# Kernel tuning notes

Hardware: AMD Instinct MI355X
Metric: run time of the kernel (lower is better)

## Reference

```python
import jax, jax.numpy as jnp
import numpy as np

B, H, L, N = 16, 256, 4096, 64


def setup_inputs() -> dict:
    key = jax.random.key(0)
    k_u, k_c, k_s = jax.random.split(key, 3)
    u = jax.random.normal(k_u, (B, H, L), dtype=jnp.float32)
    # HiPPO-style S4D-Lin init, replicated per channel
    A_re = -0.5 * jnp.ones((H, N), dtype=jnp.float32)
    A_im = jnp.pi * jnp.broadcast_to(jnp.arange(N, dtype=jnp.float32), (H, N))
    C = jax.random.normal(k_c, (H, N, 2), dtype=jnp.float32) * (0.5 ** 0.5)
    D = jnp.ones((H, 1), dtype=jnp.float32)
    log_step = jax.random.uniform(
        k_s, (H, 1), dtype=jnp.float32,
        minval=jnp.log(0.001), maxval=jnp.log(0.1))
    return {"u": u, "A_re": A_re, "A_im": A_im, "C": C, "D": D,
            "log_step": log_step}


def reference(u, A_re, A_im, C, D, log_step):
    # u: [B,H,L]; per-channel S4D params: A_* [H,N], C [H,N,2], D/log_step [H,1]
    Lq = u.shape[-1]
    step = jnp.exp(log_step)                       # [H,1]
    A = jnp.clip(A_re, None, -0.0001) + 1j * A_im  # [H,N] complex
    dtA = step * A                                 # [H,N]
    Cc = C[..., 0] + 1j * C[..., 1]                # [H,N]
    # ZOH kernel: K[h,l] = Re( sum_n C (exp(step*A)-1)/A * exp(l*step*A) )
    coef = Cc * (jnp.exp(dtA) - 1.0) / A           # [H,N]
    phase = jnp.arange(Lq)[None, :, None] * dtA[:, None, :]  # [H,L,N]
    K = jnp.einsum('hn,hln->hl', coef, jnp.exp(phase)).real  # [H,L]
    # FFT causal convolution (zero-padded to 2L)
    n = 2 * Lq
    ud = jnp.fft.rfft(u, n=n, axis=-1)             # [B,H,n//2+1]
    Kd = jnp.fft.rfft(K, n=n, axis=-1)             # [H,n//2+1]
    y = jnp.fft.irfft(ud * Kd[None], n=n, axis=-1)[..., :Lq]
    return y + D * u
```

## Files before the change

### kernel.cpp

```cpp
#include <hip/hip_runtime.h>
#include <hip/hip_bf16.h>
#include <math.h>


#define B_ 16
#define H_ 256
#define L_ 4096

typedef __attribute__((ext_vector_type(8))) short short8;
typedef __attribute__((ext_vector_type(4))) float f32x4;

#define WIN_STRIDE 72
#define TK_STRIDE  72
#define WOUT_STRIDE 136

#define WIN_ELEMS  (128 * WIN_STRIDE)
#define TK_ELEMS   (64 * TK_STRIDE)
#define WOUT_ELEMS (64 * WOUT_STRIDE)

__device__ __forceinline__ unsigned short f2bf(float f) {
    unsigned int u = __float_as_uint(f);
    u = (u + 0x7FFFu + ((u >> 16) & 1u)) >> 16;
    return (unsigned short)u;
}
__device__ __forceinline__ float bf2f(unsigned short h) {
    return __uint_as_float(((unsigned int)h) << 16);
}
__device__ __forceinline__ void split2(float v, short& hi, short& lo) {
    unsigned short h = f2bf(v);
    hi = (short)h;
    lo = (short)f2bf(v - bf2f(h));
}

__global__ __launch_bounds__(512) void s4d_tables(
    const float* __restrict__ A_re, const float* __restrict__ A_im,
    const float* __restrict__ C,    const float* __restrict__ log_step,
    unsigned short* __restrict__ win_g, unsigned short* __restrict__ tk_g,
    unsigned short* __restrict__ wout_g, float* __restrict__ lamT_g)
{
    const int bid0 = blockIdx.x;
    const int slot = bid0 >> 3;
    const int h   = (bid0 & 7) * 32 + (slot >> 4);
    const int sub = slot & 15;
    const int tid = threadIdx.x;
    __shared__ float pr[64], pi[64], cr_[64], ci_[64], Kd[64];
    __shared__ float kpart[8][64];
    const float step = expf(log_step[h]);

    if (tid < 64) {
        int n = tid;
        float are = fminf(A_re[h * 64 + n], -1e-4f);
        float aim = A_im[h * 64 + n];
        float dre = step * are, dim = step * aim;
        float er = expf(dre);
        float l1r = er * cosf(dim), l1i = er * sinf(dim);
        float inv = 1.0f / (are * are + aim * aim);
        float nre = l1r - 1.0f, nim = l1i;
        float qre = (nre * are + nim * aim) * inv;
        float qim = (nim * are - nre * aim) * inv;
        float c0 = C[(h * 64 + n) * 2], c1 = C[(h * 64 + n) * 2 + 1];
        pr[n] = dre; pi[n] = dim;
        cr_[n] = c0 * qre - c1 * qim;
        ci_[n] = c0 * qim + c1 * qre;
        if (sub == 0) {
            float m = expf(64.0f * dre);
            lamT_g[(h * 64 + n) * 2]     = m * cosf(64.0f * dim);
            lamT_g[(h * 64 + n) * 2 + 1] = m * sinf(64.0f * dim);
        }
    }
    __syncthreads();

    {
        const int d = tid & 63, q = tid >> 6;
        float acc = 0.f;
        for (int n = q * 8; n < q * 8 + 8; ++n) {
            float m = expf((float)d * pr[n]);
            float a = (float)d * pi[n];
            acc += m * (cr_[n] * cosf(a) - ci_[n] * sinf(a));
        }
        kpart[q][d] = acc;
    }
    __syncthreads();
    if (tid < 64) {
        float s01 = kpart[0][tid] + kpart[1][tid];
        float s23 = kpart[2][tid] + kpart[3][tid];
        float s45 = kpart[4][tid] + kpart[5][tid];
        float s67 = kpart[6][tid] + kpart[7][tid];
        Kd[tid] = ((s01 + s23) + s45) + s67;
    }

    unsigned short* winH = win_g + (size_t)h * (2 * WIN_ELEMS);
    unsigned short* winL = winH + WIN_ELEMS;
    for (int i = sub * 576 + tid; i < (sub + 1) * 576; i += 512) {
        int p = i / WIN_STRIDE, j = i - p * WIN_STRIDE;
        float v = 0.f;
        if (j < 64) {
            int n = p & 63;
            float e = (float)(63 - j);
            float m = expf(e * pr[n]), a = e * pi[n];
            v = (p < 64) ? m * cosf(a) : m * sinf(a);
        }
        unsigned short hv = f2bf(v);
        winH[i] = hv;
        winL[i] = f2bf(v - bf2f(hv));
    }

    unsigned short* woH = wout_g + (size_t)h * (2 * WOUT_ELEMS);
    unsigned short* woL = woH + WOUT_ELEMS;
    for (int i = sub * 544 + tid; i < (sub + 1) * 544; i += 512) {
        int j = i / WOUT_STRIDE, p = i - j * WOUT_STRIDE;
        float v = 0.f;
        if (p < 128) {
            int n = p & 63;
            float e = (float)(j + 1);
            float m = expf(e * pr[n]), a = e * pi[n];
            float lr = m * cosf(a), li = m * sinf(a);
            float wr = cr_[n] * lr - ci_[n] * li;
            float wi = cr_[n] * li + ci_[n] * lr;
            v = (p < 64) ? wr : -wi;
        }
        unsigned short hv = f2bf(v);
        woH[i] = hv;
        woL[i] = f2bf(v - bf2f(hv));
    }
    __syncthreads();

    unsigned short* tkH = tk_g + (size_t)h * (2 * TK_ELEMS);
    unsigned short* tkL = tkH + TK_ELEMS;
    for (int i = sub * 288 + tid; i < (sub + 1) * 288; i += 512) {
        int j = i / TK_STRIDE, m = i - j * TK_STRIDE;
        float v = (m < 64 && m <= j) ? Kd[j - m] : 0.f;
        unsigned short hv = f2bf(v);
        tkH[i] = hv;
        tkL[i] = f2bf(v - bf2f(hv));
    }
}

__global__ __launch_bounds__(512, 1) void s4d_main(
    const float* __restrict__ u, const float* __restrict__ D,
    const unsigned short* __restrict__ win_g, const unsigned short* __restrict__ tk_g,
    const unsigned short* __restrict__ wout_g, const float* __restrict__ lamT_g,
    float* __restrict__ y)
{
    const int tid  = threadIdx.x;
    const int lane = tid & 63, w = tid >> 6;
    const int wg   = w >> 2, ww = w & 3;
    const int l15  = lane & 15;

    const int bid  = blockIdx.x;
    const int xcd  = bid & 7, slot = bid >> 3;
    const int h  = xcd * 32 + (slot >> 3);
    const int bp = slot & 7;
    const size_t ubase0 = ((size_t)bp * H_ + h) * (size_t)L_;
    const size_t ubase1 = ((size_t)(bp + 8) * H_ + h) * (size_t)L_;

    __shared__ __align__(16) float u_lds[2][64][68];
    __shared__ __align__(16) float ES[2][64][132];
    __shared__ __align__(16) unsigned short bufB[2 * (WIN_ELEMS + TK_ELEMS)];
    unsigned short* winB  = bufB;
    unsigned short* tkB   = bufB + 2 * WIN_ELEMS;
    unsigned short* woutB = bufB;

    for (int it = 0; it < 4; ++it) {
        int l = it * 2048 + tid * 4;
        int seq = l >> 12, within = l & 4095;
        const size_t ub = seq ? ubase1 : ubase0;
        float4 v = *(const float4*)&u[ub + within];
        *(float4*)&u_lds[seq][within >> 6][within & 63] = v;
    }
    {
        const uint4* src = (const uint4*)(win_g + (size_t)h * (2 * WIN_ELEMS));
        uint4* dst = (uint4*)winB;
        for (int i = tid; i < (2 * WIN_ELEMS) / 8; i += 512) dst[i] = src[i];
    }
    {
        const uint4* src = (const uint4*)(tk_g + (size_t)h * (2 * TK_ELEMS));
        uint4* dst = (uint4*)tkB;
        for (int i = tid; i < (2 * TK_ELEMS) / 8; i += 512) dst[i] = src[i];
    }
    __syncthreads();

    const int row  = ww * 16 + l15;
    const int koff = (lane >> 4) * 8;

    short8 auh[2], aul[2];
#pragma unroll
    for (int kb = 0; kb < 2; ++kb) {
        float4 v0 = *(const float4*)&u_lds[wg][row][kb * 32 + koff];
        float4 v1 = *(const float4*)&u_lds[wg][row][kb * 32 + koff + 4];
        float vv[8] = {v0.x, v0.y, v0.z, v0.w, v1.x, v1.y, v1.z, v1.w};
#pragma unroll
        for (int e = 0; e < 8; ++e) { short hi, lo; split2(vv[e], hi, lo); auh[kb][e] = hi; aul[kb][e] = lo; }
    }

    for (int nt = 0; nt < 8; ++nt) {
        f32x4 acc = {0.f, 0.f, 0.f, 0.f};
#pragma unroll
        for (int kb = 0; kb < 2; ++kb) {
            const int boff = (nt * 16 + l15) * WIN_STRIDE + kb * 32 + koff;
            short8 bh = *(const short8*)&winB[boff];
            short8 bl = *(const short8*)&winB[WIN_ELEMS + boff];
            acc = __builtin_amdgcn_mfma_f32_16x16x32_bf16(auh[kb], bh, acc, 0, 0, 0);
            acc = __builtin_amdgcn_mfma_f32_16x16x32_bf16(aul[kb], bh, acc, 0, 0, 0);
            acc = __builtin_amdgcn_mfma_f32_16x16x32_bf16(auh[kb], bl, acc, 0, 0, 0);
        }
#pragma unroll
        for (int r = 0; r < 4; ++r)
            ES[wg][ww * 16 + (lane >> 4) * 4 + r][nt * 16 + l15] = acc[r];
    }

    f32x4 yacc[4];
    for (int nt = 0; nt < 4; ++nt) {
        f32x4 acc = {0.f, 0.f, 0.f, 0.f};
#pragma unroll
        for (int kb = 0; kb < 2; ++kb) {
            const int boff = (nt * 16 + l15) * TK_STRIDE + kb * 32 + koff;
            short8 bh = *(const short8*)&tkB[boff];
            short8 bl = *(const short8*)&tkB[TK_ELEMS + boff];
            acc = __builtin_amdgcn_mfma_f32_16x16x32_bf16(auh[kb], bh, acc, 0, 0, 0);
            acc = __builtin_amdgcn_mfma_f32_16x16x32_bf16(aul[kb], bh, acc, 0, 0, 0);
            acc = __builtin_amdgcn_mfma_f32_16x16x32_bf16(auh[kb], bl, acc, 0, 0, 0);
        }
        yacc[nt] = acc;
    }
    __syncthreads();

    if (ww == 0) {
        float ltr = lamT_g[(h * 64 + lane) * 2];
        float lti = lamT_g[(h * 64 + lane) * 2 + 1];
        float sr = 0.f, si = 0.f;
#pragma unroll 8
        for (int c = 0; c < 64; ++c) {
            float er = ES[wg][c][lane], ei = ES[wg][c][lane + 64];
            ES[wg][c][lane] = sr; ES[wg][c][lane + 64] = si;
            float nsr = ltr * sr - lti * si + er;
            si = ltr * si + lti * sr + ei;
            sr = nsr;
        }
    } else {
        const uint4* src = (const uint4*)(wout_g + (size_t)h * (2 * WOUT_ELEMS));
        uint4* dst = (uint4*)woutB;
        const int compact = (wg * 3 + (ww - 1)) * 64 + lane;
        for (int i = compact; i < (2 * WOUT_ELEMS) / 8; i += 384) dst[i] = src[i];
    }
    __syncthreads();

    for (int kb = 0; kb < 4; ++kb) {
        float4 v0 = *(const float4*)&ES[wg][row][kb * 32 + koff];
        float4 v1 = *(const float4*)&ES[wg][row][kb * 32 + koff + 4];
        float vv[8] = {v0.x, v0.y, v0.z, v0.w, v1.x, v1.y, v1.z, v1.w};
        short8 ash, asl;
#pragma unroll
        for (int e = 0; e < 8; ++e) { short hi, lo; split2(vv[e], hi, lo); ash[e] = hi; asl[e] = lo; }
#pragma unroll
        for (int nt = 0; nt < 4; ++nt) {
            const int boff = (nt * 16 + l15) * WOUT_STRIDE + kb * 32 + koff;
            short8 bh = *(const short8*)&woutB[boff];
            short8 bl = *(const short8*)&woutB[WOUT_ELEMS + boff];
            yacc[nt] = __builtin_amdgcn_mfma_f32_16x16x32_bf16(ash, bh, yacc[nt], 0, 0, 0);
            yacc[nt] = __builtin_amdgcn_mfma_f32_16x16x32_bf16(asl, bh, yacc[nt], 0, 0, 0);
            yacc[nt] = __builtin_amdgcn_mfma_f32_16x16x32_bf16(ash, bl, yacc[nt], 0, 0, 0);
        }
    }
    __syncthreads();

#pragma unroll
    for (int nt = 0; nt < 4; ++nt)
#pragma unroll
        for (int r = 0; r < 4; ++r)
            ES[wg][ww * 16 + (lane >> 4) * 4 + r][nt * 16 + l15] = yacc[nt][r];
    __syncthreads();

    const float Dh = D[h];
    for (int it = 0; it < 4; ++it) {
        int l = it * 2048 + tid * 4;
        int seq = l >> 12, within = l & 4095;
        int c = within >> 6, j = within & 63;
        float4 yv = *(const float4*)&ES[seq][c][j];
        float4 uv = *(const float4*)&u_lds[seq][c][j];
        float4 o;
        o.x = yv.x + Dh * uv.x; o.y = yv.y + Dh * uv.y;
        o.z = yv.z + Dh * uv.z; o.w = yv.w + Dh * uv.w;
        *(float4*)&y[(seq ? ubase1 : ubase0) + within] = o;
    }
}

extern "C" void kernel_launch(void* const* d_in, const int* in_sizes, int n_in,
                              void* d_out, int out_size, void* d_ws, size_t ws_size,
                              hipStream_t stream) {
    const float* u        = (const float*)d_in[0];
    const float* A_re     = (const float*)d_in[1];
    const float* A_im     = (const float*)d_in[2];
    const float* C        = (const float*)d_in[3];
    const float* D        = (const float*)d_in[4];
    const float* log_step = (const float*)d_in[5];
    float* y = (float*)d_out;

    char* ws = (char*)d_ws;
    unsigned short* win_g  = (unsigned short*)(ws);
    unsigned short* tk_g   = (unsigned short*)(ws + 9437184);
    unsigned short* wout_g = (unsigned short*)(ws + 14155776);
    float*          lamT_g = (float*)(ws + 23068672);

    s4d_tables<<<H_ * 16, 512, 0, stream>>>(A_re, A_im, C, log_step, win_g, tk_g, wout_g, lamT_g);
    s4d_main<<<(B_ * H_) / 2, 512, 0, stream>>>(u, D, win_g, tk_g, wout_g, lamT_g, y);
}
```

Before: 125.2 us.

## Fuse table generation into main kernel, computing win/tk/wout tables in LDS

```diff
diff --git a/kernel.cpp b/kernel.cpp
--- a/kernel.cpp
+++ b/kernel.cpp
@@ -32,21 +32,43 @@
     lo = (short)f2bf(v - bf2f(h));
 }
 
-__global__ __launch_bounds__(512) void s4d_tables(
+__global__ __launch_bounds__(512, 1) void s4d_main(
+    const float* __restrict__ u,
     const float* __restrict__ A_re, const float* __restrict__ A_im,
-    const float* __restrict__ C,    const float* __restrict__ log_step,
-    unsigned short* __restrict__ win_g, unsigned short* __restrict__ tk_g,
-    unsigned short* __restrict__ wout_g, float* __restrict__ lamT_g)
+    const float* __restrict__ C,    const float* __restrict__ D,
+    const float* __restrict__ log_step,
+    float* __restrict__ y)
 {
-    const int bid0 = blockIdx.x;
-    const int slot = bid0 >> 3;
-    const int h   = (bid0 & 7) * 32 + (slot >> 4);
-    const int sub = slot & 15;
-    const int tid = threadIdx.x;
+    const int tid  = threadIdx.x;
+    const int lane = tid & 63, w = tid >> 6;
+    const int wg   = w >> 2, ww = w & 3;
+    const int l15  = lane & 15;
+
+    const int bid  = blockIdx.x;
+    const int xcd  = bid & 7, slot = bid >> 3;
+    const int h  = xcd * 32 + (slot >> 3);
+    const int bp = slot & 7;
+    const size_t ubase0 = ((size_t)bp * H_ + h) * (size_t)L_;
+    const size_t ubase1 = ((size_t)(bp + 8) * H_ + h) * (size_t)L_;
+
+    __shared__ __align__(16) float u_lds[2][64][68];
+    __shared__ __align__(16) float ES[2][64][132];
+    __shared__ __align__(16) unsigned short bufB[2 * (WIN_ELEMS + TK_ELEMS)];
     __shared__ float pr[64], pi[64], cr_[64], ci_[64], Kd[64];
-    __shared__ float kpart[8][64];
+    unsigned short* winB  = bufB;
+    unsigned short* tkB   = bufB + 2 * WIN_ELEMS;
+    unsigned short* woutB = bufB;
+    float (*kpart)[64] = (float(*)[64])&ES[0][0][0];
+
+    for (int it = 0; it < 4; ++it) {
+        int l = it * 2048 + tid * 4;
+        int seq = l >> 12, within = l & 4095;
+        const size_t ub = seq ? ubase1 : ubase0;
+        float4 v = *(const float4*)&u[ub + within];
+        *(float4*)&u_lds[seq][within >> 6][within & 63] = v;
+    }
+
     const float step = expf(log_step[h]);
-
     if (tid < 64) {
         int n = tid;
         float are = fminf(A_re[h * 64 + n], -1e-4f);
@@ -62,11 +84,6 @@
         pr[n] = dre; pi[n] = dim;
         cr_[n] = c0 * qre - c1 * qim;
         ci_[n] = c0 * qim + c1 * qre;
-        if (sub == 0) {
-            float m = expf(64.0f * dre);
-            lamT_g[(h * 64 + n) * 2]     = m * cosf(64.0f * dim);
-            lamT_g[(h * 64 + n) * 2 + 1] = m * sinf(64.0f * dim);
-        }
     }
     __syncthreads();
 
@@ -89,9 +106,7 @@
         Kd[tid] = ((s01 + s23) + s45) + s67;
     }
 
-    unsigned short* winH = win_g + (size_t)h * (2 * WIN_ELEMS);
-    unsigned short* winL = winH + WIN_ELEMS;
-    for (int i = sub * 576 + tid; i < (sub + 1) * 576; i += 512) {
+    for (int i = tid; i < WIN_ELEMS; i += 512) {
         int p = i / WIN_STRIDE, j = i - p * WIN_STRIDE;
         float v = 0.f;
         if (j < 64) {
@@ -101,82 +116,17 @@
             v = (p < 64) ? m * cosf(a) : m * sinf(a);
         }
         unsigned short hv = f2bf(v);
-        winH[i] = hv;
-        winL[i] = f2bf(v - bf2f(hv));
-    }
-
-    unsigned short* woH = wout_g + (size_t)h * (2 * WOUT_ELEMS);
-    unsigned short* woL = woH + WOUT_ELEMS;
-    for (int i = sub * 544 + tid; i < (sub + 1) * 544; i += 512) {
-        int j = i / WOUT_STRIDE, p = i - j * WOUT_STRIDE;
-        float v = 0.f;
-        if (p < 128) {
-            int n = p & 63;
-            float e = (float)(j + 1);
-            float m = expf(e * pr[n]), a = e * pi[n];
-            float lr = m * cosf(a), li = m * sinf(a);
-            float wr = cr_[n] * lr - ci_[n] * li;
-            float wi = cr_[n] * li + ci_[n] * lr;
-            v = (p < 64) ? wr : -wi;
-        }
-        unsigned short hv = f2bf(v);
-        woH[i] = hv;
-        woL[i] = f2bf(v - bf2f(hv));
-    }
-    __syncthreads();
-
-    unsigned short* tkH = tk_g + (size_t)h * (2 * TK_ELEMS);
-    unsigned short* tkL = tkH + TK_ELEMS;
-    for (int i = sub * 288 + tid; i < (sub + 1) * 288; i += 512) {
+        winB[i] = hv;
+        winB[WIN_ELEMS + i] = f2bf(v - bf2f(hv));
+    }
+    __syncthreads();
+
+    for (int i = tid; i < TK_ELEMS; i += 512) {
         int j = i / TK_STRIDE, m = i - j * TK_STRIDE;
         float v = (m < 64 && m <= j) ? Kd[j - m] : 0.f;
         unsigned short hv = f2bf(v);
-        tkH[i] = hv;
-        tkL[i] = f2bf(v - bf2f(hv));
-    }
-}
-
-__global__ __launch_bounds__(512, 1) void s4d_main(
-    const float* __restrict__ u, const float* __restrict__ D,
-    const unsigned short* __restrict__ win_g, const unsigned short* __restrict__ tk_g,
-    const unsigned short* __restrict__ wout_g, const float* __restrict__ lamT_g,
-    float* __restrict__ y)
-{
-    const int tid  = threadIdx.x;
-    const int lane = tid & 63, w = tid >> 6;
-    const int wg   = w >> 2, ww = w & 3;
-    const int l15  = lane & 15;
-
-    const int bid  = blockIdx.x;
-    const int xcd  = bid & 7, slot = bid >> 3;
-    const int h  = xcd * 32 + (slot >> 3);
-    const int bp = slot & 7;
-    const size_t ubase0 = ((size_t)bp * H_ + h) * (size_t)L_;
-    const size_t ubase1 = ((size_t)(bp + 8) * H_ + h) * (size_t)L_;
-
-    __shared__ __align__(16) float u_lds[2][64][68];
-    __shared__ __align__(16) float ES[2][64][132];
-    __shared__ __align__(16) unsigned short bufB[2 * (WIN_ELEMS + TK_ELEMS)];
-    unsigned short* winB  = bufB;
-    unsigned short* tkB   = bufB + 2 * WIN_ELEMS;
-    unsigned short* woutB = bufB;
-
-    for (int it = 0; it < 4; ++it) {
-        int l = it * 2048 + tid * 4;
-        int seq = l >> 12, within = l & 4095;
-        const size_t ub = seq ? ubase1 : ubase0;
-        float4 v = *(const float4*)&u[ub + within];
-        *(float4*)&u_lds[seq][within >> 6][within & 63] = v;
-    }
-    {
-        const uint4* src = (const uint4*)(win_g + (size_t)h * (2 * WIN_ELEMS));
-        uint4* dst = (uint4*)winB;
-        for (int i = tid; i < (2 * WIN_ELEMS) / 8; i += 512) dst[i] = src[i];
-    }
-    {
-        const uint4* src = (const uint4*)(tk_g + (size_t)h * (2 * TK_ELEMS));
-        uint4* dst = (uint4*)tkB;
-        for (int i = tid; i < (2 * TK_ELEMS) / 8; i += 512) dst[i] = src[i];
+        tkB[i] = hv;
+        tkB[TK_ELEMS + i] = f2bf(v - bf2f(hv));
     }
     __syncthreads();
 
@@ -226,8 +176,9 @@
     __syncthreads();
 
     if (ww == 0) {
-        float ltr = lamT_g[(h * 64 + lane) * 2];
-        float lti = lamT_g[(h * 64 + lane) * 2 + 1];
+        float lm  = expf(64.0f * pr[lane]);
+        float ltr = lm * cosf(64.0f * pi[lane]);
+        float lti = lm * sinf(64.0f * pi[lane]);
         float sr = 0.f, si = 0.f;
 #pragma unroll 8
         for (int c = 0; c < 64; ++c) {
@@ -238,10 +189,23 @@
             sr = nsr;
         }
     } else {
-        const uint4* src = (const uint4*)(wout_g + (size_t)h * (2 * WOUT_ELEMS));
-        uint4* dst = (uint4*)woutB;
         const int compact = (wg * 3 + (ww - 1)) * 64 + lane;
-        for (int i = compact; i < (2 * WOUT_ELEMS) / 8; i += 384) dst[i] = src[i];
+        for (int i = compact; i < WOUT_ELEMS; i += 384) {
+            int j = i / WOUT_STRIDE, p = i - j * WOUT_STRIDE;
+            float v = 0.f;
+            if (p < 128) {
+                int n = p & 63;
+                float e = (float)(j + 1);
+                float m = expf(e * pr[n]), a = e * pi[n];
+                float lr = m * cosf(a), li = m * sinf(a);
+                float wr = cr_[n] * lr - ci_[n] * li;
+                float wi = cr_[n] * li + ci_[n] * lr;
+                v = (p < 64) ? wr : -wi;
+            }
+            unsigned short hv = f2bf(v);
+            woutB[i] = hv;
+            woutB[WOUT_ELEMS + i] = f2bf(v - bf2f(hv));
+        }
     }
     __syncthreads();
 
@@ -296,12 +260,5 @@
     const float* log_step = (const float*)d_in[5];
     float* y = (float*)d_out;
 
-    char* ws = (char*)d_ws;
-    unsigned short* win_g  = (unsigned short*)(ws);
-    unsigned short* tk_g   = (unsigned short*)(ws + 9437184);
-    unsigned short* wout_g = (unsigned short*)(ws + 14155776);
-    float*          lamT_g = (float*)(ws + 23068672);
-
-    s4d_tables<<<H_ * 16, 512, 0, stream>>>(A_re, A_im, C, log_step, win_g, tk_g, wout_g, lamT_g);
-    s4d_main<<<(B_ * H_) / 2, 512, 0, stream>>>(u, D, win_g, tk_g, wout_g, lamT_g, y);
-}
+    s4d_main<<<(B_ * H_) / 2, 512, 0, stream>>>(u, A_re, A_im, C, D, log_step, y);
+}
```

New measurement: 190.7 us. 1.52x slower.
